# Kernel optimization log

Measured on AMD Instinct MI355X. Metric: run time of the kernel, lower is better.

Reference implementation:

```python
import jax, jax.numpy as jnp
import numpy as np

D_MODEL = 1024
N_HIDDEN = 64   # per-head dim (outer factor of packed proj dim)
N_HEAD = 16
B, L = 2, 2048


def setup_inputs() -> dict:
    key = jax.random.key(0)
    ks = jax.random.split(key, 7)
    s = 0.02
    return {
        "q": jax.random.normal(ks[0], (B, L, D_MODEL), dtype=jnp.float32),
        "k": jax.random.normal(ks[1], (B, L, D_MODEL), dtype=jnp.float32),
        "v": jax.random.normal(ks[2], (B, L, D_MODEL), dtype=jnp.float32),
        # torch nn.Linear weights: shape (out_features, in_features), y = x @ W.T
        "W_Q": jax.random.normal(ks[3], (N_HIDDEN * N_HEAD, D_MODEL), dtype=jnp.float32) * s,
        "W_K": jax.random.normal(ks[4], (N_HIDDEN * N_HEAD, D_MODEL), dtype=jnp.float32) * s,
        "W_V": jax.random.normal(ks[5], (N_HIDDEN * N_HEAD, D_MODEL), dtype=jnp.float32) * s,
        "W_O": jax.random.normal(ks[6], (D_MODEL, N_HEAD * N_HIDDEN), dtype=jnp.float32) * s,
    }


def reference(q, k, v, W_Q, W_K, W_V, W_O):
    b, l, _ = q.shape
    # projections (bias=False)
    qp = q @ W_Q.T  # [b,l,n_hidden*n_head]
    kp = k @ W_K.T
    vp = v @ W_V.T
    # rearrange 'b l (c h) -> b l c h' with c=n_hidden: hidden is OUTER factor
    qh = qp.reshape(b, l, N_HIDDEN, N_HEAD)
    kh = kp.reshape(b, l, N_HIDDEN, N_HEAD)
    vh = vp.reshape(b, l, N_HIDDEN, N_HEAD)
    scores = jnp.einsum('bldh,bjdh->bhlj', qh, kh) / np.float32(np.sqrt(N_HIDDEN))
    attn = jax.nn.softmax(scores, axis=-1)
    out = jnp.einsum('bhlj,bjdh->bldh', attn, vh)  # [b,l,n_hidden,n_head]
    out = out.reshape(b, l, N_HIDDEN * N_HEAD)      # 'b l d h -> b l (d h)'
    return out @ W_O.T
```

## Files before the change

kernel.cpp:

```cpp
#include <hip/hip_runtime.h>
#include <hip/hip_bf16.h>
#include <stdint.h>

typedef __attribute__((ext_vector_type(8))) short short8;
typedef __attribute__((ext_vector_type(4))) float f32x4;
typedef __attribute__((ext_vector_type(16))) float f32x16;
typedef __attribute__((ext_vector_type(2))) int int2v;
typedef unsigned short u16;
typedef unsigned int u32;


#define WAIT_VM12() do { asm volatile("s_waitcnt vmcnt(12)" ::: "memory"); \
                         __builtin_amdgcn_sched_barrier(0); } while (0)
#define WAIT_VM8()  do { asm volatile("s_waitcnt vmcnt(8)" ::: "memory"); \
                         __builtin_amdgcn_sched_barrier(0); } while (0)
#define WAIT_VM0()  do { asm volatile("s_waitcnt vmcnt(0)" ::: "memory"); \
                         __builtin_amdgcn_sched_barrier(0); } while (0)
#define BARRIER()   do { __builtin_amdgcn_s_barrier(); \
                         __builtin_amdgcn_sched_barrier(0); } while (0)
#define LGKM0_BAR() do { asm volatile("s_waitcnt lgkmcnt(0)" ::: "memory"); \
                         __builtin_amdgcn_s_barrier(); \
                         __builtin_amdgcn_sched_barrier(0); } while (0)

#define FSWZ(r) (((r) ^ ((r) >> 3)) & 7)

__device__ __forceinline__ u16 bf16rne(float f) {
  u32 u = __builtin_bit_cast(u32, f);
  u += 0x7FFFu + ((u >> 16) & 1u);
  return (u16)(u >> 16);
}

__device__ __forceinline__ u32 cvtpk(float lo, float hi) {
  u32 r;
  asm("v_cvt_pk_bf16_f32 %0, %1, %2" : "=v"(r) : "v"(lo), "v"(hi));
  return r;
}

__device__ __forceinline__ void gl_lds16(const u16* g, u16* l) {
  __builtin_amdgcn_global_load_lds((const __attribute__((address_space(1))) void*)g,
                                   (__attribute__((address_space(3))) void*)l, 16, 0, 0);
}

struct CastArgs {
  const float* src[4];
  u16* dst[4];
  int n4[4];
};

__global__ void cast_all(CastArgs a) {
  const int id = blockIdx.y;
  const float* __restrict__ s = a.src[id];
  u16* __restrict__ d = a.dst[id];
  const int stride = gridDim.x * blockDim.x;
  const int i0 = blockIdx.x * blockDim.x + threadIdx.x;
  if (id < 3) {
    const int n4 = a.n4[id];
    for (int i = i0; i < n4; i += stride) {
      float4 v = ((const float4*)s)[i];
      u32 lo = (u32)bf16rne(v.x) | ((u32)bf16rne(v.y) << 16);
      u32 hi = (u32)bf16rne(v.z) | ((u32)bf16rne(v.w) << 16);
      ((uint2*)d)[i] = make_uint2(lo, hi);
    }
  } else {
    const int n = a.n4[3];
    for (int i = i0; i < n; i += stride) {
      int row = i >> 10, c = i & 1023;
      int hh = c >> 6, dd = c & 63;
      d[i] = bf16rne(s[(row << 10) + dd * 16 + hh]);
    }
  }
}

struct ProjFArgs { const float* A[3]; const u16* W[3]; u16* D[3]; float scale[3]; };

__global__ __launch_bounds__(256, 2) void gemm_projf(ProjFArgs pa) {
  const int bid = blockIdx.x;
  const int grp = ((bid >> 6) << 3) | (bid & 7);
  const int bn = ((bid >> 3) & 7) * 128;
  const int z = grp >> 5;
  const int bm = (grp & 31) * 128;
  const float* __restrict__ A = pa.A[z];
  const u16* __restrict__ Bw = pa.W[z];
  u16* __restrict__ D = pa.D[z];
  const float ascale = pa.scale[z];
  const int epi = (z == 2) ? 1 : 0;

  const int tid = threadIdx.x, lane = tid & 63, w = tid >> 6;
  const int wr = w >> 1, wc = w & 1;
  __shared__ __align__(16) u16 As[128 * 64];
  __shared__ __align__(16) u16 Bs[2][128 * 64];

  f32x4 acc[4][4];
#pragma unroll
  for (int m = 0; m < 4; ++m)
#pragma unroll
    for (int n = 0; n < 4; ++n) acc[m][n] = (f32x4){0.f, 0.f, 0.f, 0.f};

  struct ARegs { float4 v[8]; };
  ARegs RA, RB;

  auto STAGE_A = [&](int kt, ARegs& R) {
#pragma unroll
    for (int i = 0; i < 4; ++i) {
      int c = tid + i * 256;
      int row = c >> 3;
      int col = (((c & 7) ^ (row & 7)) << 3);
      const float* src = A + (size_t)(bm + row) * 1024 + kt * 64 + col;
      R.v[2 * i] = *(const float4*)(src);
      R.v[2 * i + 1] = *(const float4*)(src + 4);
    }
  };
  auto WRITE_A = [&](ARegs& R) {
#pragma unroll
    for (int i = 0; i < 4; ++i) {
      int c = tid + i * 256;
      u32 p0 = (u32)bf16rne(R.v[2 * i].x) | ((u32)bf16rne(R.v[2 * i].y) << 16);
      u32 p1 = (u32)bf16rne(R.v[2 * i].z) | ((u32)bf16rne(R.v[2 * i].w) << 16);
      u32 p2 = (u32)bf16rne(R.v[2 * i + 1].x) | ((u32)bf16rne(R.v[2 * i + 1].y) << 16);
      u32 p3 = (u32)bf16rne(R.v[2 * i + 1].z) | ((u32)bf16rne(R.v[2 * i + 1].w) << 16);
      *(uint4*)&As[c * 8] = make_uint4(p0, p1, p2, p3);
    }
  };
  auto STAGE_B = [&](int kt, int b) {
#pragma unroll
    for (int i = 0; i < 4; ++i) {
      int c = tid + i * 256;
      int row = c >> 3;
      int swz = (((c & 7) ^ (row & 7)) << 3);
      gl_lds16(Bw + (size_t)(bn + row) * 1024 + kt * 64 + swz, &Bs[b][c * 8]);
    }
  };
  auto COMPUTE = [&](int b) {
#pragma unroll
    for (int ks = 0; ks < 2; ++ks) {
      const int ck = ks * 4 + (lane >> 4);
      short8 af[4], bfr[4];
#pragma unroll
      for (int m = 0; m < 4; ++m) {
        int r = wr * 64 + m * 16 + (lane & 15);
        af[m] = *(const short8*)&As[(r * 8 + (ck ^ (r & 7))) * 8];
      }
#pragma unroll
      for (int n = 0; n < 4; ++n) {
        int r = wc * 64 + n * 16 + (lane & 15);
        bfr[n] = *(const short8*)&Bs[b][(r * 8 + (ck ^ (r & 7))) * 8];
      }
#pragma unroll
      for (int m = 0; m < 4; ++m)
#pragma unroll
        for (int n = 0; n < 4; ++n)
          acc[m][n] = __builtin_amdgcn_mfma_f32_16x16x32_bf16(af[m], bfr[n], acc[m][n], 0, 0, 0);
    }
  };

  STAGE_A(0, RA); STAGE_B(0, 0);
  STAGE_A(1, RB); STAGE_B(1, 1);
  for (int kt = 0; kt < 16; ++kt) {
    if (kt < 14) { WAIT_VM12(); } else { WAIT_VM0(); }
    if (kt & 1) WRITE_A(RB); else WRITE_A(RA);
    LGKM0_BAR();
    COMPUTE(kt & 1);
    BARRIER();
    if (kt < 14) {
      if (kt & 1) STAGE_A(kt + 2, RB); else STAGE_A(kt + 2, RA);
      STAGE_B(kt + 2, kt & 1);
    }
  }

  const int lrow4 = (lane >> 4) << 2;
  const int h = lane & 15;
  if (epi == 0) {
    const int dbase = (bn + wc * 64) >> 4;
#pragma unroll
    for (int m = 0; m < 4; ++m)
#pragma unroll
      for (int i = 0; i < 4; ++i) {
        int R = bm + wr * 64 + m * 16 + lrow4 + i;
        int b = R >> 11, l = R & 2047;
        u32 lo = (u32)bf16rne(acc[m][0][i] * ascale) | ((u32)bf16rne(acc[m][1][i] * ascale) << 16);
        u32 hi = (u32)bf16rne(acc[m][2][i] * ascale) | ((u32)bf16rne(acc[m][3][i] * ascale) << 16);
        size_t addr = ((size_t)((b * 16 + h) * 2048 + l)) * 64 + dbase;
        *(uint2*)(D + addr) = make_uint2(lo, hi);
      }
  } else {
    const int dbase = (bn + wc * 64) >> 4;
    const int b = bm >> 11;
#pragma unroll
    for (int m = 0; m < 4; ++m) {
      int l0 = (bm & 2047) + wr * 64 + m * 16 + lrow4;
#pragma unroll
      for (int n = 0; n < 4; ++n) {
        int d = dbase + n;
        u32 lo = (u32)bf16rne(acc[m][n][0]) | ((u32)bf16rne(acc[m][n][1]) << 16);
        u32 hi = (u32)bf16rne(acc[m][n][2]) | ((u32)bf16rne(acc[m][n][3]) << 16);
        size_t addr = ((size_t)((b * 16 + h) * 64 + d)) * 2048 + l0;
        *(uint2*)(D + addr) = make_uint2(lo, hi);
      }
    }
  }
}

__global__ __launch_bounds__(256, 2) void gemm_oproj(const u16* __restrict__ A,
                                                     const u16* __restrict__ Bw,
                                                     float* __restrict__ C) {
  const int bid = blockIdx.x;
  const int slot = bid >> 3;
  const int bm = ((bid & 7) * 4 + (slot >> 3)) * 128;
  const int bn = (slot & 7) * 128;
  const int tid = threadIdx.x, lane = tid & 63, w = tid >> 6;
  const int wr = w >> 1, wc = w & 1;
  __shared__ __align__(16) u16 As[2][128 * 64];
  __shared__ __align__(16) u16 Bs[2][128 * 64];
  f32x4 acc[4][4];
#pragma unroll
  for (int m = 0; m < 4; ++m)
#pragma unroll
    for (int n = 0; n < 4; ++n) acc[m][n] = (f32x4){0.f, 0.f, 0.f, 0.f};

  auto STAGE = [&](int kt, int b) {
#pragma unroll
    for (int i = 0; i < 4; ++i) {
      int c = tid + i * 256;
      int row = c >> 3, kc = c & 7;
      int swz = (kc ^ (row & 7)) << 3;
      int bA = bm >> 11;
      int lrow = (bm & 2047) + row;
      const u16* srcA = A + ((size_t)(bA * 16 + kt) * 2048 + lrow) * 64 + swz;
      gl_lds16(srcA, &As[b][c * 8]);
      const u16* srcB = Bw + (size_t)(bn + row) * 1024 + kt * 64 + swz;
      gl_lds16(srcB, &Bs[b][c * 8]);
    }
  };

  auto COMPUTE = [&](int b) {
#pragma unroll
    for (int ks = 0; ks < 2; ++ks) {
      const int ck = ks * 4 + (lane >> 4);
      short8 af[4], bfr[4];
#pragma unroll
      for (int m = 0; m < 4; ++m) {
        int r = wr * 64 + m * 16 + (lane & 15);
        af[m] = *(const short8*)&As[b][(r * 8 + (ck ^ (r & 7))) * 8];
      }
#pragma unroll
      for (int n = 0; n < 4; ++n) {
        int r = wc * 64 + n * 16 + (lane & 15);
        bfr[n] = *(const short8*)&Bs[b][(r * 8 + (ck ^ (r & 7))) * 8];
      }
#pragma unroll
      for (int m = 0; m < 4; ++m)
#pragma unroll
        for (int n = 0; n < 4; ++n)
          acc[m][n] = __builtin_amdgcn_mfma_f32_16x16x32_bf16(af[m], bfr[n], acc[m][n], 0, 0, 0);
    }
  };

  STAGE(0, 0);
  STAGE(1, 1);
  for (int kt = 0; kt < 15; ++kt) {
    WAIT_VM8();
    BARRIER();
    COMPUTE(kt & 1);
    BARRIER();
    if (kt < 14) STAGE(kt + 2, kt & 1);
  }
  WAIT_VM0();
  BARRIER();
  COMPUTE(1);

  const int lrow4 = (lane >> 4) << 2;
#pragma unroll
  for (int m = 0; m < 4; ++m)
#pragma unroll
    for (int i = 0; i < 4; ++i) {
      int R = bm + wr * 64 + m * 16 + lrow4 + i;
      size_t base = (size_t)R * 1024 + bn + wc * 64 + (lane & 15);
#pragma unroll
      for (int n = 0; n < 4; ++n) C[base + n * 16] = acc[m][n][i];
    }
}

__global__ __launch_bounds__(128, 2) void attn_kernel(const u16* __restrict__ Qh,
                                                      const u16* __restrict__ Kh,
                                                      const u16* __restrict__ Vt,
                                                      u16* __restrict__ Oh) {
  const int hb = blockIdx.x;
  const int qt = blockIdx.y;
  const int tid = threadIdx.x, lane = tid & 63, w = tid >> 6;
  const int l31 = lane & 31, hi = lane >> 5;
  __shared__ __align__(16) u16 Ks[2][64 * 64];
  __shared__ __align__(16) u16 Vs[3][64 * 64];

  const u16* Qg = Qh + (size_t)hb * (2048 * 64);
  const u16* Kg = Kh + (size_t)hb * (2048 * 64);
  const u16* Vg = Vt + (size_t)hb * (64 * 2048);
  const int qrow = qt * 64 + w * 32 + l31;

  short8 qf[4];
#pragma unroll
  for (int ks = 0; ks < 4; ++ks)
    qf[ks] = *(const short8*)(Qg + (size_t)qrow * 64 + ks * 16 + hi * 8);

  int rs[4], sw[4];
#pragma unroll
  for (int i = 0; i < 4; ++i) {
    int c = tid + i * 128;
    rs[i] = c >> 3;
    sw[i] = (((c & 7) ^ FSWZ(rs[i])) << 3);
  }

  auto STAGE_K = [&](int t, int slot) {
    const size_t ko = (size_t)t * (64 * 64);
#pragma unroll
    for (int i = 0; i < 4; ++i) {
      int c = tid + i * 128;
      gl_lds16(Kg + ko + (size_t)rs[i] * 64 + sw[i], &Ks[slot][c * 8]);
    }
  };
  auto STAGE_V = [&](int t, int slot) {
    const int vo = t * 64;
#pragma unroll
    for (int i = 0; i < 4; ++i) {
      int c = tid + i * 128;
      gl_lds16(Vg + (size_t)rs[i] * 2048 + vo + sw[i], &Vs[slot][c * 8]);
    }
  };

  f32x16 oacc0, oacc1, SA0, SA1, SB0, SB1;
#pragma unroll
  for (int i = 0; i < 16; ++i) { oacc0[i] = 0.f; oacc1[i] = 0.f; }
  u32 pkA[16], pkB[16];
  float lrow = 0.f;

  auto QKT = [&](int kslot, f32x16& s0, f32x16& s1) {
#pragma unroll
    for (int i = 0; i < 16; ++i) { s0[i] = 0.f; s1[i] = 0.f; }
    __builtin_amdgcn_s_setprio(1);
#pragma unroll
    for (int ks = 0; ks < 4; ++ks) {
      const int ck = 2 * ks + hi;
      const int r0 = l31, r1 = 32 + l31;
      short8 k0 = *(const short8*)&Ks[kslot][(r0 * 8 + (ck ^ FSWZ(r0))) * 8];
      short8 k1 = *(const short8*)&Ks[kslot][(r1 * 8 + (ck ^ FSWZ(r1))) * 8];
      s0 = __builtin_amdgcn_mfma_f32_32x32x16_bf16(k0, qf[ks], s0, 0, 0, 0);
      s1 = __builtin_amdgcn_mfma_f32_32x32x16_bf16(k1, qf[ks], s1, 0, 0, 0);
    }
    __builtin_amdgcn_s_setprio(0);
  };

  auto PV = [&](const u32* pk, int vslot) {
    __builtin_amdgcn_s_setprio(1);
#pragma unroll
    for (int c = 0; c < 4; ++c) {
      union { u32 wu[4]; short8 v; } un;
      un.wu[0] = pk[c * 4 + 0]; un.wu[1] = pk[c * 4 + 1];
      un.wu[2] = pk[c * 4 + 2]; un.wu[3] = pk[c * 4 + 3];
      const int ckv = 2 * c + hi;
      const int rv0 = l31, rv1 = 32 + l31;
      short8 v0 = *(const short8*)&Vs[vslot][(rv0 * 8 + (ckv ^ FSWZ(rv0))) * 8];
      short8 v1 = *(const short8*)&Vs[vslot][(rv1 * 8 + (ckv ^ FSWZ(rv1))) * 8];
      oacc0 = __builtin_amdgcn_mfma_f32_32x32x16_bf16(v0, un.v, oacc0, 0, 0, 0);
      oacc1 = __builtin_amdgcn_mfma_f32_32x32x16_bf16(v1, un.v, oacc1, 0, 0, 0);
    }
    __builtin_amdgcn_s_setprio(0);
  };

  auto SOFTMAX = [&](f32x16& s0, f32x16& s1, u32* pk) {
#pragma unroll
    for (int i = 0; i < 16; ++i) {
      s0[i] = __builtin_amdgcn_exp2f(s0[i]);
      s1[i] = __builtin_amdgcn_exp2f(s1[i]);
    }
    f32x16 a01 = s0 + s1;
    float r8[8];
#pragma unroll
    for (int i = 0; i < 8; ++i) r8[i] = a01[i] + a01[i + 8];
#pragma unroll
    for (int i = 0; i < 4; ++i) r8[i] += r8[i + 4];
    float rsum = (r8[0] + r8[1]) + (r8[2] + r8[3]);
    int2v pr = __builtin_amdgcn_permlane32_swap(__builtin_bit_cast(int, rsum),
                                                __builtin_bit_cast(int, rsum), false, false);
    lrow += __builtin_bit_cast(float, pr[0]) + __builtin_bit_cast(float, pr[1]);
#pragma unroll
    for (int c = 0; c < 4; ++c) {
      float pe0, pe1, pe2, pe3, pe4, pe5, pe6, pe7;
      if (c < 2) {
        const int s8 = (c & 1) * 8;
        pe0 = s0[s8 + 0]; pe1 = s0[s8 + 1]; pe2 = s0[s8 + 2]; pe3 = s0[s8 + 3];
        pe4 = s0[s8 + 4]; pe5 = s0[s8 + 5]; pe6 = s0[s8 + 6]; pe7 = s0[s8 + 7];
      } else {
        const int s8 = (c & 1) * 8;
        pe0 = s1[s8 + 0]; pe1 = s1[s8 + 1]; pe2 = s1[s8 + 2]; pe3 = s1[s8 + 3];
        pe4 = s1[s8 + 4]; pe5 = s1[s8 + 5]; pe6 = s1[s8 + 6]; pe7 = s1[s8 + 7];
      }
      u32 a0 = cvtpk(pe0, pe1), a1 = cvtpk(pe2, pe3);
      u32 a2 = cvtpk(pe4, pe5), a3 = cvtpk(pe6, pe7);
      int2v w02 = __builtin_amdgcn_permlane32_swap((int)a0, (int)a2, false, false);
      int2v w13 = __builtin_amdgcn_permlane32_swap((int)a1, (int)a3, false, false);
      pk[c * 4 + 0] = (u32)w02[0]; pk[c * 4 + 1] = (u32)w13[0];
      pk[c * 4 + 2] = (u32)w02[1]; pk[c * 4 + 3] = (u32)w13[1];
    }
  };

  STAGE_K(0, 0); STAGE_K(1, 1); STAGE_V(0, 0);
  WAIT_VM8(); BARRIER();
  QKT(0, SA0, SA1);
  BARRIER();
  STAGE_K(2, 0); STAGE_V(1, 1);
  WAIT_VM8(); BARRIER();
  QKT(1, SB0, SB1);
  SOFTMAX(SA0, SA1, pkB);
  BARRIER();
  STAGE_K(3, 1); STAGE_V(2, 2);

  for (int i = 2; i < 32; i += 2) {
    WAIT_VM8(); BARRIER();
    QKT(0, SA0, SA1);
    PV(pkB, (i - 2) % 3);
    SOFTMAX(SB0, SB1, pkA);
    BARRIER();
    if (i + 2 <= 31) STAGE_K(i + 2, 0);
    STAGE_V(i + 1, (i + 1) % 3);
    WAIT_VM8(); BARRIER();
    QKT(1, SB0, SB1);
    PV(pkA, (i - 1) % 3);
    SOFTMAX(SA0, SA1, pkB);
    BARRIER();
    if (i + 3 <= 31) STAGE_K(i + 3, 1);
    if (i + 2 <= 31) STAGE_V(i + 2, (i + 2) % 3);
  }

  WAIT_VM0(); BARRIER();
  SOFTMAX(SB0, SB1, pkA);
  PV(pkB, 30 % 3);
  PV(pkA, 31 % 3);

  const float inv = 1.0f / lrow;
  u16* Og = Oh + (size_t)hb * (2048 * 64) + (size_t)qrow * 64;
#pragma unroll
  for (int dblk = 0; dblk < 2; ++dblk) {
#pragma unroll
    for (int r = 0; r < 16; r += 2) {
      const int d = dblk * 32 + (r & 3) + 8 * (r >> 2) + 4 * hi;
      float v0 = (dblk ? oacc1[r] : oacc0[r]) * inv;
      float v1 = (dblk ? oacc1[r + 1] : oacc0[r + 1]) * inv;
      *(u32*)(Og + d) = (u32)bf16rne(v0) | ((u32)bf16rne(v1) << 16);
    }
  }
}

extern "C" void kernel_launch(void* const* d_in, const int* in_sizes, int n_in,
                              void* d_out, int out_size, void* d_ws, size_t ws_size,
                              hipStream_t stream) {
  const float* q = (const float*)d_in[0];
  const float* k = (const float*)d_in[1];
  const float* v = (const float*)d_in[2];
  const float* WQ = (const float*)d_in[3];
  const float* WK = (const float*)d_in[4];
  const float* WV = (const float*)d_in[5];
  const float* WO = (const float*)d_in[6];
  float* out = (float*)d_out;
  char* ws = (char*)d_ws;
  const size_t MB = 1024 * 1024;
  if (ws_size < 64 * MB) return;

  u16* WQb = (u16*)(ws + 24 * MB);
  u16* WKb = (u16*)(ws + 26 * MB);
  u16* WVb = (u16*)(ws + 28 * MB);
  u16* WOt = (u16*)(ws + 30 * MB);
  u16* Qh  = (u16*)(ws + 32 * MB);
  u16* Kh  = (u16*)(ws + 40 * MB);
  u16* Vt  = (u16*)(ws + 48 * MB);
  u16* Ohd = (u16*)(ws + 56 * MB);

  CastArgs ca;
  ca.src[0] = WQ; ca.dst[0] = WQb; ca.n4[0] = (1024 * 1024) / 4;
  ca.src[1] = WK; ca.dst[1] = WKb; ca.n4[1] = (1024 * 1024) / 4;
  ca.src[2] = WV; ca.dst[2] = WVb; ca.n4[2] = (1024 * 1024) / 4;
  ca.src[3] = WO; ca.dst[3] = WOt; ca.n4[3] = 1024 * 1024;
  cast_all<<<dim3(128, 4), 256, 0, stream>>>(ca);

  ProjFArgs pa;
  pa.A[0] = q; pa.W[0] = WQb; pa.D[0] = Qh;  pa.scale[0] = 0.18033688011f;
  pa.A[1] = k; pa.W[1] = WKb; pa.D[1] = Kh;  pa.scale[1] = 1.0f;
  pa.A[2] = v; pa.W[2] = WVb; pa.D[2] = Vt;  pa.scale[2] = 1.0f;
  gemm_projf<<<768, 256, 0, stream>>>(pa);

  attn_kernel<<<dim3(32, 32), 128, 0, stream>>>(Qh, Kh, Vt, Ohd);

  gemm_oproj<<<256, 256, 0, stream>>>(Ohd, WOt, out);
}
```

Baseline: 145.6 us.

## Rewrite QKV projection GEMM with 256x256 tiles and 8-wave quadrant-interleaved pipeline

Replaces the 128x128 fused-fp32 QKV projection GEMM with a 256x256-tile kernel using 512 threads and 192 blocks. Each k-step is split into four quadrant phases that interleave LDS reads, fp32 A loads with bf16 conversion, B direct-to-LDS loads and MFMA, with s_setprio raised around the MFMA bursts. The aim is more operand reuse per loaded byte and better overlap of memory with compute. In exchange, 192 blocks leave many CUs idle, register pressure is higher, and the epilogue issues narrower 32-bit stores for the Q/K layout.

```diff
diff --git a/kernel.cpp b/kernel.cpp
--- a/kernel.cpp
+++ b/kernel.cpp
@@ -10,9 +10,11 @@
 typedef unsigned int u32;
 
 
-#define WAIT_VM12() do { asm volatile("s_waitcnt vmcnt(12)" ::: "memory"); \
+#define WAIT_VM8()  do { asm volatile("s_waitcnt vmcnt(8)" ::: "memory"); \
                          __builtin_amdgcn_sched_barrier(0); } while (0)
-#define WAIT_VM8()  do { asm volatile("s_waitcnt vmcnt(8)" ::: "memory"); \
+#define WAIT_VM6()  do { asm volatile("s_waitcnt vmcnt(6)" ::: "memory"); \
+                         __builtin_amdgcn_sched_barrier(0); } while (0)
+#define WAIT_VM4()  do { asm volatile("s_waitcnt vmcnt(4)" ::: "memory"); \
                          __builtin_amdgcn_sched_barrier(0); } while (0)
 #define WAIT_VM0()  do { asm volatile("s_waitcnt vmcnt(0)" ::: "memory"); \
                          __builtin_amdgcn_sched_barrier(0); } while (0)
@@ -73,128 +75,184 @@
 
 struct ProjFArgs { const float* A[3]; const u16* W[3]; u16* D[3]; float scale[3]; };
 
-__global__ __launch_bounds__(256, 2) void gemm_projf(ProjFArgs pa) {
+#define PH_MFMA(P)                                                             \
+  do {                                                                         \
+    __builtin_amdgcn_s_setprio(1);                                             \
+    _Pragma("unroll") for (int ks = 0; ks < 2; ++ks)                           \
+      _Pragma("unroll") for (int m = 0; m < 4; ++m)                            \
+        _Pragma("unroll") for (int n = 0; n < 2; ++n)                          \
+          acc[P][m][n] = __builtin_amdgcn_mfma_f32_16x16x32_bf16(              \
+              af[ks][m], bf[ks][n], acc[P][m][n], 0, 0, 0);                    \
+    __builtin_amdgcn_s_setprio(0);                                             \
+  } while (0)
+
+__global__ __launch_bounds__(512, 2) void gemm_proj256(ProjFArgs pa) {
   const int bid = blockIdx.x;
-  const int grp = ((bid >> 6) << 3) | (bid & 7);
-  const int bn = ((bid >> 3) & 7) * 128;
-  const int z = grp >> 5;
-  const int bm = (grp & 31) * 128;
+  const int x = bid & 7;
+  const int rr = bid >> 3;
+  const int bn = (rr & 3) * 256;
+  const int g = (rr >> 2) * 8 + x;
+  const int z = g >> 4;
+  const int bm = (g & 15) * 256;
   const float* __restrict__ A = pa.A[z];
   const u16* __restrict__ Bw = pa.W[z];
   u16* __restrict__ D = pa.D[z];
   const float ascale = pa.scale[z];
-  const int epi = (z == 2) ? 1 : 0;
 
   const int tid = threadIdx.x, lane = tid & 63, w = tid >> 6;
-  const int wr = w >> 1, wc = w & 1;
-  __shared__ __align__(16) u16 As[128 * 64];
-  __shared__ __align__(16) u16 Bs[2][128 * 64];
-
-  f32x4 acc[4][4];
-#pragma unroll
-  for (int m = 0; m < 4; ++m)
-#pragma unroll
-    for (int n = 0; n < 4; ++n) acc[m][n] = (f32x4){0.f, 0.f, 0.f, 0.f};
-
-  struct ARegs { float4 v[8]; };
-  ARegs RA, RB;
-
-  auto STAGE_A = [&](int kt, ARegs& R) {
-#pragma unroll
-    for (int i = 0; i < 4; ++i) {
-      int c = tid + i * 256;
-      int row = c >> 3;
-      int col = (((c & 7) ^ (row & 7)) << 3);
-      const float* src = A + (size_t)(bm + row) * 1024 + kt * 64 + col;
-      R.v[2 * i] = *(const float4*)(src);
-      R.v[2 * i + 1] = *(const float4*)(src + 4);
-    }
-  };
-  auto WRITE_A = [&](ARegs& R) {
-#pragma unroll
-    for (int i = 0; i < 4; ++i) {
-      int c = tid + i * 256;
-      u32 p0 = (u32)bf16rne(R.v[2 * i].x) | ((u32)bf16rne(R.v[2 * i].y) << 16);
-      u32 p1 = (u32)bf16rne(R.v[2 * i].z) | ((u32)bf16rne(R.v[2 * i].w) << 16);
-      u32 p2 = (u32)bf16rne(R.v[2 * i + 1].x) | ((u32)bf16rne(R.v[2 * i + 1].y) << 16);
-      u32 p3 = (u32)bf16rne(R.v[2 * i + 1].z) | ((u32)bf16rne(R.v[2 * i + 1].w) << 16);
-      *(uint4*)&As[c * 8] = make_uint4(p0, p1, p2, p3);
-    }
-  };
-  auto STAGE_B = [&](int kt, int b) {
-#pragma unroll
-    for (int i = 0; i < 4; ++i) {
-      int c = tid + i * 256;
-      int row = c >> 3;
-      int swz = (((c & 7) ^ (row & 7)) << 3);
-      gl_lds16(Bw + (size_t)(bn + row) * 1024 + kt * 64 + swz, &Bs[b][c * 8]);
-    }
-  };
-  auto COMPUTE = [&](int b) {
+  const int wr2 = w >> 2, wc4 = w & 3;
+  const int l15 = lane & 15, l4 = lane >> 4;
+
+  __shared__ __align__(16) u16 As[2][2][8192];
+  __shared__ __align__(16) u16 Bs[2][2][8192];
+
+  f32x4 acc[4][4][2];
+#pragma unroll
+  for (int p = 0; p < 4; ++p)
+#pragma unroll
+    for (int m = 0; m < 4; ++m)
+#pragma unroll
+      for (int n = 0; n < 2; ++n) acc[p][m][n] = (f32x4){0.f, 0.f, 0.f, 0.f};
+
+  struct AR { float4 v[4]; };
+  AR Rn0, Rc1;
+
+  auto STAGE_B = [&](int kt, int half, int db) {
+#pragma unroll
+    for (int i = 0; i < 2; ++i) {
+      int idx = tid + i * 512;
+      int row = idx >> 3, kc = idx & 7;
+      gl_lds16(Bw + (size_t)(bn + half * 128 + row) * 1024 + kt * 64 + ((kc ^ (row & 7)) << 3),
+               &Bs[db][half][idx * 8]);
+    }
+  };
+  auto LOAD_A = [&](int kt, int half, AR& R) {
+#pragma unroll
+    for (int i = 0; i < 2; ++i) {
+      int idx = tid + i * 512;
+      int row = idx >> 3, kc = idx & 7;
+      const float* s = A + (size_t)(bm + half * 128 + row) * 1024 + kt * 64 + ((kc ^ (row & 7)) << 3);
+      R.v[2 * i] = *(const float4*)s;
+      R.v[2 * i + 1] = *(const float4*)(s + 4);
+    }
+  };
+  auto WRITE_A = [&](int half, int db, AR& R) {
+#pragma unroll
+    for (int i = 0; i < 2; ++i) {
+      int idx = tid + i * 512;
+      u32 q0 = (u32)bf16rne(R.v[2 * i].x) | ((u32)bf16rne(R.v[2 * i].y) << 16);
+      u32 q1 = (u32)bf16rne(R.v[2 * i].z) | ((u32)bf16rne(R.v[2 * i].w) << 16);
+      u32 q2 = (u32)bf16rne(R.v[2 * i + 1].x) | ((u32)bf16rne(R.v[2 * i + 1].y) << 16);
+      u32 q3 = (u32)bf16rne(R.v[2 * i + 1].z) | ((u32)bf16rne(R.v[2 * i + 1].w) << 16);
+      *(uint4*)&As[db][half][idx * 8] = make_uint4(q0, q1, q2, q3);
+    }
+  };
+
+  short8 af[2][4], bf[2][2];
+  auto READ_A = [&](int half, int d) {
 #pragma unroll
     for (int ks = 0; ks < 2; ++ks) {
-      const int ck = ks * 4 + (lane >> 4);
-      short8 af[4], bfr[4];
+      const int ck = ks * 4 + l4;
 #pragma unroll
       for (int m = 0; m < 4; ++m) {
-        int r = wr * 64 + m * 16 + (lane & 15);
-        af[m] = *(const short8*)&As[(r * 8 + (ck ^ (r & 7))) * 8];
+        int r = wr2 * 64 + m * 16 + l15;
+        af[ks][m] = *(const short8*)&As[d][half][(r * 8 + (ck ^ (r & 7))) * 8];
       }
-#pragma unroll
-      for (int n = 0; n < 4; ++n) {
-        int r = wc * 64 + n * 16 + (lane & 15);
-        bfr[n] = *(const short8*)&Bs[b][(r * 8 + (ck ^ (r & 7))) * 8];
+    }
+  };
+  auto READ_B = [&](int half, int d) {
+#pragma unroll
+    for (int ks = 0; ks < 2; ++ks) {
+      const int ck = ks * 4 + l4;
+#pragma unroll
+      for (int n = 0; n < 2; ++n) {
+        int r = wc4 * 32 + n * 16 + l15;
+        bf[ks][n] = *(const short8*)&Bs[d][half][(r * 8 + (ck ^ (r & 7))) * 8];
       }
+    }
+  };
+
+  LOAD_A(0, 0, Rn0);
+  STAGE_B(0, 0, 0);
+  STAGE_B(0, 1, 0);
+  LOAD_A(0, 1, Rc1);
+  WAIT_VM8();
+  WRITE_A(0, 0, Rn0);
+
+  for (int t = 0; t < 15; ++t) {
+    const int d = t & 1, nd = d ^ 1;
+    WAIT_VM6();
+    LGKM0_BAR();
+    READ_A(0, d);
+    READ_B(0, d);
+    LOAD_A(t + 1, 0, Rn0);
+    PH_MFMA(0);
+    WAIT_VM4();
+    BARRIER();
+    READ_B(1, d);
+    WRITE_A(1, d, Rc1);
+    STAGE_B(t + 1, 0, nd);
+    PH_MFMA(1);
+    LGKM0_BAR();
+    READ_A(1, d);
+    STAGE_B(t + 1, 1, nd);
+    PH_MFMA(2);
+    WAIT_VM4();
+    READ_B(0, d);
+    WRITE_A(0, nd, Rn0);
+    LOAD_A(t + 1, 1, Rc1);
+    PH_MFMA(3);
+  }
+  {
+    const int d = 1;
+    WAIT_VM6();
+    LGKM0_BAR();
+    READ_A(0, d);
+    READ_B(0, d);
+    PH_MFMA(0);
+    WAIT_VM0();
+    BARRIER();
+    READ_B(1, d);
+    WRITE_A(1, d, Rc1);
+    PH_MFMA(1);
+    LGKM0_BAR();
+    READ_A(1, d);
+    PH_MFMA(2);
+    READ_B(0, d);
+    PH_MFMA(3);
+  }
+
+  if (z != 2) {
+    const int dbase = (bn >> 4) + wc4 * 2;
+#pragma unroll
+    for (int p = 0; p < 4; ++p) {
+      const int mq = p >> 1, nq = (p == 1 || p == 2) ? 1 : 0;
 #pragma unroll
       for (int m = 0; m < 4; ++m)
 #pragma unroll
-        for (int n = 0; n < 4; ++n)
-          acc[m][n] = __builtin_amdgcn_mfma_f32_16x16x32_bf16(af[m], bfr[n], acc[m][n], 0, 0, 0);
-    }
-  };
-
-  STAGE_A(0, RA); STAGE_B(0, 0);
-  STAGE_A(1, RB); STAGE_B(1, 1);
-  for (int kt = 0; kt < 16; ++kt) {
-    if (kt < 14) { WAIT_VM12(); } else { WAIT_VM0(); }
-    if (kt & 1) WRITE_A(RB); else WRITE_A(RA);
-    LGKM0_BAR();
-    COMPUTE(kt & 1);
-    BARRIER();
-    if (kt < 14) {
-      if (kt & 1) STAGE_A(kt + 2, RB); else STAGE_A(kt + 2, RA);
-      STAGE_B(kt + 2, kt & 1);
-    }
-  }
-
-  const int lrow4 = (lane >> 4) << 2;
-  const int h = lane & 15;
-  if (epi == 0) {
-    const int dbase = (bn + wc * 64) >> 4;
-#pragma unroll
-    for (int m = 0; m < 4; ++m)
-#pragma unroll
-      for (int i = 0; i < 4; ++i) {
-        int R = bm + wr * 64 + m * 16 + lrow4 + i;
-        int b = R >> 11, l = R & 2047;
-        u32 lo = (u32)bf16rne(acc[m][0][i] * ascale) | ((u32)bf16rne(acc[m][1][i] * ascale) << 16);
-        u32 hi = (u32)bf16rne(acc[m][2][i] * ascale) | ((u32)bf16rne(acc[m][3][i] * ascale) << 16);
-        size_t addr = ((size_t)((b * 16 + h) * 2048 + l)) * 64 + dbase;
-        *(uint2*)(D + addr) = make_uint2(lo, hi);
-      }
+        for (int i = 0; i < 4; ++i) {
+          int R = bm + mq * 128 + wr2 * 64 + m * 16 + l4 * 4 + i;
+          int b = R >> 11, l = R & 2047;
+          u32 pk = (u32)bf16rne(acc[p][m][0][i] * ascale) |
+                   ((u32)bf16rne(acc[p][m][1][i] * ascale) << 16);
+          *(u32*)(D + ((size_t)((b * 16 + l15) * 2048 + l)) * 64 + dbase + nq * 8) = pk;
+        }
+    }
   } else {
-    const int dbase = (bn + wc * 64) >> 4;
     const int b = bm >> 11;
 #pragma unroll
-    for (int m = 0; m < 4; ++m) {
-      int l0 = (bm & 2047) + wr * 64 + m * 16 + lrow4;
-#pragma unroll
-      for (int n = 0; n < 4; ++n) {
-        int d = dbase + n;
-        u32 lo = (u32)bf16rne(acc[m][n][0]) | ((u32)bf16rne(acc[m][n][1]) << 16);
-        u32 hi = (u32)bf16rne(acc[m][n][2]) | ((u32)bf16rne(acc[m][n][3]) << 16);
-        size_t addr = ((size_t)((b * 16 + h) * 64 + d)) * 2048 + l0;
-        *(uint2*)(D + addr) = make_uint2(lo, hi);
+    for (int p = 0; p < 4; ++p) {
+      const int mq = p >> 1, nq = (p == 1 || p == 2) ? 1 : 0;
+#pragma unroll
+      for (int m = 0; m < 4; ++m) {
+        int l0 = (bm & 2047) + mq * 128 + wr2 * 64 + m * 16 + l4 * 4;
+#pragma unroll
+        for (int n = 0; n < 2; ++n) {
+          int dv = (bn >> 4) + nq * 8 + wc4 * 2 + n;
+          u32 lo = (u32)bf16rne(acc[p][m][n][0]) | ((u32)bf16rne(acc[p][m][n][1]) << 16);
+          u32 hi = (u32)bf16rne(acc[p][m][n][2]) | ((u32)bf16rne(acc[p][m][n][3]) << 16);
+          *(uint2*)(D + ((size_t)((b * 16 + l15) * 64 + dv)) * 2048 + l0) = make_uint2(lo, hi);
+        }
       }
     }
   }
@@ -484,7 +542,7 @@
   pa.A[0] = q; pa.W[0] = WQb; pa.D[0] = Qh;  pa.scale[0] = 0.18033688011f;
   pa.A[1] = k; pa.W[1] = WKb; pa.D[1] = Kh;  pa.scale[1] = 1.0f;
   pa.A[2] = v; pa.W[2] = WVb; pa.D[2] = Vt;  pa.scale[2] = 1.0f;
-  gemm_projf<<<768, 256, 0, stream>>>(pa);
+  gemm_proj256<<<192, 512, 0, stream>>>(pa);
 
   attn_kernel<<<dim3(32, 32), 128, 0, stream>>>(Qh, Kh, Vt, Ohd);
 
```

After: 142.7 us. -2.0%, faster.
